# Performance work log

Measured on AMD Instinct MI355X. Metric: run time of the kernel, lower is better.

## Reference

```python
import jax, jax.numpy as jnp
import numpy as np

WIN, STRIDE = 8, 4          # unfold(-1, 8, 4) in FIDSubsequence.forward
HID, FEAT = 128, 30         # action2motion FID classifier: GRU hidden 128, lin1 -> 30
GAMMA = 1.0                 # SoftDTW default gamma
INF = 1e10


def _windows(xyz):
    x = xyz[0]                                   # (J, 3, T)
    T = x.shape[-1]
    nw = (T - WIN) // STRIDE + 1
    idx = jnp.arange(nw)[:, None] * STRIDE + jnp.arange(WIN)[None, :]
    w = x[:, :, idx]
    seq = w.transpose(3, 2, 0, 1)
    return seq.reshape(WIN, nw, -1)


def _gru_layer(xs, Wih, Whh, bih, bhh):
    # xs: (T, B, in); torch GRU gate order r, z, n
    H = Whh.shape[1]
    def step(h, x):
        gi = x @ Wih.T + bih
        gh = h @ Whh.T + bhh
        ir, iz, i_n = jnp.split(gi, 3, -1)
        hr, hz, h_n = jnp.split(gh, 3, -1)
        r = jax.nn.sigmoid(ir + hr)
        z = jax.nn.sigmoid(iz + hz)
        n = jnp.tanh(i_n + r * h_n)
        h_new = (1.0 - z) * n + z * h
        return h_new, h_new
    h0 = jnp.zeros((xs.shape[1], H), xs.dtype)
    _, hs = jax.lax.scan(step, h0, xs)
    return hs                                    # (T, B, H)


def _feats(xyz, Wih1, Whh1, bih1, bhh1, Wih2, Whh2, bih2, bhh2, W1, b1):
    # Batched equivalent of the per-window classifier loop in distance()
    seq = _windows(xyz)                          # (8, nw, 72)
    h1 = _gru_layer(seq, Wih1, Whh1, bih1, bhh1)
    h2 = _gru_layer(h1, Wih2, Whh2, bih2, bhh2)
    return h2[-1] @ W1.T + b1                    # (nw, 30) -- lengths=8 == full window


def _pairwise_sqdist(f1, f2):
    # ((f1 - f2) ** 2).sum(-1) without materializing (n, m, d)
    d = (f1 * f1).sum(-1)[:, None] + (f2 * f2).sum(-1)[None, :] - 2.0 * (f1 @ f2.T)
    return jnp.maximum(d, 0.0)


def _softdtw(D, gamma):
    # anti-diagonal wavefront: A_k[i] = R[i, k-i]
    n, m = D.shape
    rows = jnp.arange(n)
    def step(carry, k):
        A2, A1 = carry
        j = k - rows
        valid = (j >= 0) & (j < m)
        d = D[rows, jnp.clip(j, 0, m - 1)]
        diag = jnp.concatenate([jnp.where(k == 0, 0.0, INF)[None], A2[:-1]])
        up = jnp.concatenate([jnp.full((1,), INF, D.dtype), A1[:-1]])
        smin = -gamma * jax.nn.logsumexp(-jnp.stack([diag, up, A1]) / gamma, axis=0)
        newA = jnp.where(valid, d + smin, INF)
        return (A1, newA), None
    A = jnp.full((n,), INF, D.dtype)
    (_, last), _ = jax.lax.scan(step, (A, A), jnp.arange(n + m - 1))
    return last[-1]                              # R[n-1, m-1]


def setup_inputs() -> dict:
    key = jax.random.key(0)
    ks = jax.random.split(key, 12)
    T, J, IN = 8196, 24, 72
    s = 1.0 / np.sqrt(HID)
    f32 = jnp.float32
    return {
        "x_xyz": jax.random.normal(ks[0], (1, J, 3, T), f32),
        "y_xyz": jax.random.normal(ks[1], (1, J, 3, T), f32),
        "Wih1": jax.random.uniform(ks[2], (3 * HID, IN), f32, -s, s),
        "Whh1": jax.random.uniform(ks[3], (3 * HID, HID), f32, -s, s),
        "bih1": jax.random.uniform(ks[4], (3 * HID,), f32, -s, s),
        "bhh1": jax.random.uniform(ks[5], (3 * HID,), f32, -s, s),
        "Wih2": jax.random.uniform(ks[6], (3 * HID, HID), f32, -s, s),
        "Whh2": jax.random.uniform(ks[7], (3 * HID, HID), f32, -s, s),
        "bih2": jax.random.uniform(ks[8], (3 * HID,), f32, -s, s),
        "bhh2": jax.random.uniform(ks[9], (3 * HID,), f32, -s, s),
        "W1": jax.random.uniform(ks[10], (FEAT, HID), f32, -s, s),
        "b1": jax.random.uniform(ks[11], (FEAT,), f32, -s, s),
    }


def reference(x_xyz, y_xyz, Wih1, Whh1, bih1, bhh1, Wih2, Whh2, bih2, bhh2, W1, b1):
    f1 = _feats(x_xyz, Wih1, Whh1, bih1, bhh1, Wih2, Whh2, bih2, bhh2, W1, b1)
    f2 = _feats(y_xyz, Wih1, Whh1, bih1, bhh1, Wih2, Whh2, bih2, bhh2, W1, b1)
    D = _pairwise_sqdist(f1, f2)                 # (nw, nw)
    return jnp.reshape(_softdtw(D, GAMMA), (1,))
```

## Files before the change

### kernel.cpp

```cpp
#include <hip/hip_runtime.h>
#include <stdint.h>

#define T_LEN 8196
#define LOG2E 1.4426950408889634f
#define LN2   0.6931471805599453f
#define INF2  1.4426950e10f
#define PD_LD 2080
#define PD_OFF 16

__device__ __forceinline__ float fexp2(float x) {
#if __has_builtin(__builtin_amdgcn_exp2f)
    return __builtin_amdgcn_exp2f(x);
#else
    return __expf(x * LN2);
#endif
}
__device__ __forceinline__ float flog2(float x) {
#if __has_builtin(__builtin_amdgcn_logf)
    return __builtin_amdgcn_logf(x);
#else
    return __logf(x) * LOG2E;
#endif
}
__device__ __forceinline__ float sigm(float x) { return 1.0f / (1.0f + __expf(-x)); }
__device__ __forceinline__ float tanh_f(float x) {
    x = fminf(fmaxf(x, -15.0f), 15.0f);
    float e = __expf(2.0f * x);
    return (e - 1.0f) / (e + 1.0f);
}

__global__ void k_prep(const float* __restrict__ Wih1, const float* __restrict__ Whh1,
                       const float* __restrict__ Wih2, const float* __restrict__ Whh2,
                       float* __restrict__ wt) {
    int gid = blockIdx.x * 256 + threadIdx.x;
    if (gid >= 175104) return;
    const float* src;
    int r, K;
    if (gid < 27648)       { r = gid;          K = 72;  src = Wih1; }
    else if (gid < 76800)  { r = gid - 27648;  K = 128; src = Whh1; }
    else if (gid < 125952) { r = gid - 76800;  K = 128; src = Wih2; }
    else                   { r = gid - 125952; K = 128; src = Whh2; }
    int kc   = r / 1536;
    int rem  = r - kc * 1536;
    int gate = rem >> 9;
    int rem2 = rem & 511;
    int u    = rem2 >> 2;
    int ki   = rem2 & 3;
    wt[gid] = src[(gate * 128 + u) * K + kc * 4 + ki];
}

__global__ __launch_bounds__(256)
void k_gru(const float* __restrict__ X, const float* __restrict__ Y,
           const float* __restrict__ wt,
           const float* __restrict__ bih1, const float* __restrict__ bhh1,
           const float* __restrict__ bih2, const float* __restrict__ bhh2,
           const float* __restrict__ W1, const float* __restrict__ b1,
           float* __restrict__ fbuf) {
    __shared__ __align__(16) float xb[72 * 12];
    __shared__ __align__(16) float h1l[128 * 12];
    __shared__ __align__(16) float h2l[128 * 12];

    const int tid = threadIdx.x;
    const int u = tid & 127;
    const int w0 = (tid >> 7) * 4;
    const int bx = blockIdx.x;
    const int seq = bx >> 8;
    const int wbase = (bx & 255) << 3;
    const float* xp = seq ? Y : X;

    const float* wih1 = wt;
    const float* whh1 = wt + 27648;
    const float* wih2 = wt + 76800;
    const float* whh2 = wt + 125952;
    const int u4 = u << 2;

    const float br1  = bih1[u] + bhh1[u];
    const float bz1  = bih1[128 + u] + bhh1[128 + u];
    const float bni1 = bih1[256 + u];
    const float bnh1 = bhh1[256 + u];
    const float br2  = bih2[u] + bhh2[u];
    const float bz2  = bih2[128 + u] + bhh2[128 + u];
    const float bni2 = bih2[256 + u];
    const float bnh2 = bhh2[256 + u];

    float h1r[4], h2r[4];
#pragma unroll
    for (int j = 0; j < 4; ++j) { h1r[j] = 0.f; h2r[j] = 0.f; }
    for (int e = tid; e < 128 * 12; e += 256) { h1l[e] = 0.f; h2l[e] = 0.f; }
    __syncthreads();

    for (int t = 0; t < 8; ++t) {
        for (int e = tid; e < 72 * 8; e += 256) {
            int k = e >> 3, w = e & 7;
            int jj = k / 3, c = k - jj * 3;
            xb[k * 12 + w] = xp[jj * (3 * T_LEN) + c * T_LEN + ((wbase + w) << 2) + t];
        }
        __syncthreads();

        float ar[4], az[4], ai[4], ah[4];
#pragma unroll
        for (int j = 0; j < 4; ++j) { ar[j] = br1; az[j] = bz1; ai[j] = bni1; ah[j] = bnh1; }
#pragma unroll 1
        for (int kc = 0; kc < 18; ++kc) {
            const float4 wr4 = *(const float4*)&wih1[kc * 1536 + u4];
            const float4 wz4 = *(const float4*)&wih1[kc * 1536 + 512 + u4];
            const float4 wn4 = *(const float4*)&wih1[kc * 1536 + 1024 + u4];
            const float wrk[4] = {wr4.x, wr4.y, wr4.z, wr4.w};
            const float wzk[4] = {wz4.x, wz4.y, wz4.z, wz4.w};
            const float wnk[4] = {wn4.x, wn4.y, wn4.z, wn4.w};
#pragma unroll
            for (int ki = 0; ki < 4; ++ki) {
                const float4 x0 = *(const float4*)&xb[(kc * 4 + ki) * 12 + w0];
                float xv[4] = {x0.x, x0.y, x0.z, x0.w};
#pragma unroll
                for (int j = 0; j < 4; ++j) {
                    ar[j] = fmaf(wrk[ki], xv[j], ar[j]);
                    az[j] = fmaf(wzk[ki], xv[j], az[j]);
                    ai[j] = fmaf(wnk[ki], xv[j], ai[j]);
                }
            }
        }
#pragma unroll 1
        for (int kc = 0; kc < 32; ++kc) {
            const float4 wr4 = *(const float4*)&whh1[kc * 1536 + u4];
            const float4 wz4 = *(const float4*)&whh1[kc * 1536 + 512 + u4];
            const float4 wn4 = *(const float4*)&whh1[kc * 1536 + 1024 + u4];
            const float wrk[4] = {wr4.x, wr4.y, wr4.z, wr4.w};
            const float wzk[4] = {wz4.x, wz4.y, wz4.z, wz4.w};
            const float wnk[4] = {wn4.x, wn4.y, wn4.z, wn4.w};
#pragma unroll
            for (int ki = 0; ki < 4; ++ki) {
                const float4 x0 = *(const float4*)&h1l[(kc * 4 + ki) * 12 + w0];
                float xv[4] = {x0.x, x0.y, x0.z, x0.w};
#pragma unroll
                for (int j = 0; j < 4; ++j) {
                    ar[j] = fmaf(wrk[ki], xv[j], ar[j]);
                    az[j] = fmaf(wzk[ki], xv[j], az[j]);
                    ah[j] = fmaf(wnk[ki], xv[j], ah[j]);
                }
            }
        }
        __syncthreads();
#pragma unroll
        for (int j = 0; j < 4; ++j) {
            float r = sigm(ar[j]);
            float z = sigm(az[j]);
            float n = tanh_f(ai[j] + r * ah[j]);
            h1r[j] = (1.f - z) * n + z * h1r[j];
        }
#pragma unroll
        for (int j = 0; j < 4; ++j) h1l[u * 12 + w0 + j] = h1r[j];
        __syncthreads();

#pragma unroll
        for (int j = 0; j < 4; ++j) { ar[j] = br2; az[j] = bz2; ai[j] = bni2; ah[j] = bnh2; }
#pragma unroll 1
        for (int kc = 0; kc < 32; ++kc) {
            const float4 wr4 = *(const float4*)&wih2[kc * 1536 + u4];
            const float4 wz4 = *(const float4*)&wih2[kc * 1536 + 512 + u4];
            const float4 wn4 = *(const float4*)&wih2[kc * 1536 + 1024 + u4];
            const float wrk[4] = {wr4.x, wr4.y, wr4.z, wr4.w};
            const float wzk[4] = {wz4.x, wz4.y, wz4.z, wz4.w};
            const float wnk[4] = {wn4.x, wn4.y, wn4.z, wn4.w};
#pragma unroll
            for (int ki = 0; ki < 4; ++ki) {
                const float4 x0 = *(const float4*)&h1l[(kc * 4 + ki) * 12 + w0];
                float xv[4] = {x0.x, x0.y, x0.z, x0.w};
#pragma unroll
                for (int j = 0; j < 4; ++j) {
                    ar[j] = fmaf(wrk[ki], xv[j], ar[j]);
                    az[j] = fmaf(wzk[ki], xv[j], az[j]);
                    ai[j] = fmaf(wnk[ki], xv[j], ai[j]);
                }
            }
        }
#pragma unroll 1
        for (int kc = 0; kc < 32; ++kc) {
            const float4 wr4 = *(const float4*)&whh2[kc * 1536 + u4];
            const float4 wz4 = *(const float4*)&whh2[kc * 1536 + 512 + u4];
            const float4 wn4 = *(const float4*)&whh2[kc * 1536 + 1024 + u4];
            const float wrk[4] = {wr4.x, wr4.y, wr4.z, wr4.w};
            const float wzk[4] = {wz4.x, wz4.y, wz4.z, wz4.w};
            const float wnk[4] = {wn4.x, wn4.y, wn4.z, wn4.w};
#pragma unroll
            for (int ki = 0; ki < 4; ++ki) {
                const float4 x0 = *(const float4*)&h2l[(kc * 4 + ki) * 12 + w0];
                float xv[4] = {x0.x, x0.y, x0.z, x0.w};
#pragma unroll
                for (int j = 0; j < 4; ++j) {
                    ar[j] = fmaf(wrk[ki], xv[j], ar[j]);
                    az[j] = fmaf(wzk[ki], xv[j], az[j]);
                    ah[j] = fmaf(wnk[ki], xv[j], ah[j]);
                }
            }
        }
        __syncthreads();
#pragma unroll
        for (int j = 0; j < 4; ++j) {
            float r = sigm(ar[j]);
            float z = sigm(az[j]);
            float n = tanh_f(ai[j] + r * ah[j]);
            h2r[j] = (1.f - z) * n + z * h2r[j];
        }
#pragma unroll
        for (int j = 0; j < 4; ++j) h2l[u * 12 + w0 + j] = h2r[j];
        __syncthreads();
    }

    for (int idx = tid; idx < 8 * 30; idx += 256) {
        int w = idx / 30, ff = idx - w * 30;
        float acc = b1[ff];
        for (int k = 0; k < 128; ++k) acc = fmaf(h2l[k * 12 + w], W1[ff * 128 + k], acc);
        fbuf[(seq * 2048 + wbase + w) * 32 + ff] = acc;
    }
}

__global__ __launch_bounds__(256)
void k_pair(const float* __restrict__ fbuf, float* __restrict__ Ep) {
    __shared__ float f1t[64 * 33];
    __shared__ float f2t[64 * 33];
    const int tid = threadIdx.x;
    const int i0 = blockIdx.y * 64, j0 = blockIdx.x * 64;
    for (int e = tid; e < 64 * 32; e += 256) {
        int r = e >> 5, c = e & 31;
        f1t[r * 33 + c] = fbuf[(i0 + r) * 32 + c];
        f2t[r * 33 + c] = fbuf[(2048 + j0 + r) * 32 + c];
    }
    __syncthreads();
    const int tx = tid & 15, ty = tid >> 4;
    float acc[4][4];
#pragma unroll
    for (int r = 0; r < 4; ++r)
#pragma unroll
        for (int c = 0; c < 4; ++c) acc[r][c] = 0.f;
    for (int k = 0; k < 30; ++k) {
        float a[4], b[4];
#pragma unroll
        for (int r = 0; r < 4; ++r) a[r] = f1t[(ty * 4 + r) * 33 + k];
#pragma unroll
        for (int c = 0; c < 4; ++c) b[c] = f2t[(tx * 4 + c) * 33 + k];
#pragma unroll
        for (int r = 0; r < 4; ++r)
#pragma unroll
            for (int c = 0; c < 4; ++c) {
                float d = a[r] - b[c];
                acc[r][c] = fmaf(d, d, acc[r][c]);
            }
    }
#pragma unroll
    for (int r = 0; r < 4; ++r) {
        float4 v = make_float4(__expf(-acc[r][0]), __expf(-acc[r][1]),
                               __expf(-acc[r][2]), __expf(-acc[r][3]));
        *(float4*)&Ep[(size_t)(i0 + ty * 4 + r) * PD_LD + PD_OFF + j0 + tx * 4] = v;
    }
}

#define DTW_GROUP(G, CT)                                                         \
  {                                                                              \
    float inA, inB, dgl;                                                         \
    if (lane == 0) {                                                             \
        inA = sIn[2 * (G)]; inB = sIn[2 * (G) + 1];                              \
        dgl = ((G) == 0) ? carryA : sIn[2 * (G) - 1];                            \
    } else { inA = pA; inB = pB; dgl = dgPrev; }                                 \
    {                                              \
        float mnG = fminf(fminf(inA, inB), dgl);                                 \
        float lim = mnG + 100.f;                                                 \
        if (Sc > lim) {                                                          \
            int ddg = (int)fmaxf(lim - Sc, -2.0e9f);                             \
            W0 = ldexpf(W0, ddg); W1 = ldexpf(W1, ddg);                          \
            W2 = ldexpf(W2, ddg); W3 = ldexpf(W3, ddg);                          \
            Sc = lim;                                                            \
        }                                                                        \
    }                                                                            \
    float ua = fexp2(Sc - inA);                                                  \
    float ub = fexp2(Sc - inB);                                                  \
    float da = fexp2(Sc - dgl);                                                  \
    float eA0 = CT[0][2*(G)],   eA1 = CT[1][2*(G)];                              \
    float eA2 = CT[2][2*(G)],   eA3 = CT[3][2*(G)];                              \
    float eB0 = CT[0][2*(G)+1], eB1 = CT[1][2*(G)+1];                            \
    float eB2 = CT[2][2*(G)+1], eB3 = CT[3][2*(G)+1];                            \
    float oA0 = eA0 * (da + W0);                                                 \
    float oA1 = eA1 * (W0 + W1);                                                 \
    float oA2 = eA2 * (W1 + W2);                                                 \
    float oA3 = eA3 * (W2 + W3);                                                 \
    float a0 = fmaf(eA0, ua, oA0);                                               \
    float a1 = fmaf(eA1, a0, oA1);                                               \
    float a2 = fmaf(eA2, a1, oA2);                                               \
    float a3 = fmaf(eA3, a2, oA3);                                               \
    float oB0 = eB0 * (ua + a0);                                                 \
    float oB1 = eB1 * (a0 + a1);                                                 \
    float oB2 = eB2 * (a1 + a2);                                                 \
    float oB3 = eB3 * (a2 + a3);                                                 \
    float b0 = fmaf(eB0, ub, oB0);                                               \
    float b1 = fmaf(eB1, b0, oB1);                                               \
    float b2 = fmaf(eB2, b1, oB2);                                               \
    float b3 = fmaf(eB3, b2, oB3);                                               \
    W0 = b0; W1 = b1; W2 = b2; W3 = b3;                                          \
    float blogA = fminf(Sc - flog2(a3), INF2);                                   \
    float blogB = fminf(Sc - flog2(b3), INF2);                                   \
    blog[2 * (G)] = blogA; blog[2 * (G) + 1] = blogB;                            \
    float sA = __shfl_up(blogA, 1);                                              \
    float sB = __shfl_up(blogB, 1);                                              \
    dgPrev = pB; pA = sA; pB = sB;                                               \
    mnAcc = fminf(mnAcc, fminf(sA, sB));                                         \
  }

#define DTW_MACRO(CUR, PF, PVC, PVI, M)                                          \
  {                                                                              \
    const int m = (M);                                                           \
    {       \
        int bs = 8 * (m + 2) - 2 * lane;                                         \
        bs = bs < -16 ? -16 : (bs > 2048 ? 2048 : bs);                           \
        _Pragma("unroll")                                                        \
        for (int r = 0; r < 4; ++r) {                                            \
            _Pragma("unroll")                                                    \
            for (int h = 0; h < 4; ++h) {                                        \
                float2 v = *(const float2*)(rp[r] + bs + 2 * h);                 \
                PF[r][2 * h] = v.x; PF[r][2 * h + 1] = v.y;                      \
            }                                                                    \
        }                                                                        \
    }                                                                            \
    if (b > 0 && lane == 0) {            \
        _Pragma("unroll")                                                        \
        for (int u = 0; u < 8; ++u) {                                            \
            int jc = 8 * (m + 3) + u; jc = jc > 2047 ? 2047 : jc;                \
            PVI[u] = __hip_atomic_load(&bIn[jc], __ATOMIC_RELAXED,               \
                                       __HIP_MEMORY_SCOPE_AGENT);                \
        }                                                                        \
    }                                                                            \
    float blog[8];                                                               \
    float mnAcc = INF2;                                                          \
    DTW_GROUP(0, CUR) DTW_GROUP(1, CUR) DTW_GROUP(2, CUR) DTW_GROUP(3, CUR)      \
    carryA = sIn[7];                                                             \
    if (lane == 63) {                                                            \
        if (b < 7) {                                                             \
            _Pragma("unroll")                                                    \
            for (int c = 0; c < 8; ++c) {                                        \
                int j = 8 * m + c - 126;                                         \
                if (j >= 0 && j < 2048) {                                        \
                    uint64_t pk = ((uint64_t)(uint32_t)j << 32) |                \
                                  (uint64_t)__float_as_uint(blog[c]);            \
                    (void)__hip_atomic_exchange(&bOut[j], pk, __ATOMIC_RELAXED,  \
                                                __HIP_MEMORY_SCOPE_AGENT);       \
                }                                                                \
            }                                                                    \
        } else if (m == 271) {                      \
            res = blog[5];                                                       \
        }                                                                        \
    }                                                                            \
    if (b > 0 && lane == 0) {      \
        bool again = false;                                                      \
        _Pragma("unroll")                                                        \
        for (int u = 0; u < 8; ++u) {                                            \
            int jc = 8 * (m + 1) + u; jc = jc > 2047 ? 2047 : jc;                \
            if ((uint32_t)(PVC[u] >> 32) != (uint32_t)jc) again = true;          \
        }                                                                        \
        while (again) {              \
            __builtin_amdgcn_s_sleep(2);                                         \
            _Pragma("unroll")                                                    \
            for (int u = 0; u < 8; ++u) {                                        \
                int jc = 8 * (m + 1) + u; jc = jc > 2047 ? 2047 : jc;            \
                PVC[u] = __hip_atomic_load(&bIn[jc], __ATOMIC_RELAXED,           \
                                           __HIP_MEMORY_SCOPE_AGENT);            \
            }                                                                    \
            again = false;                                                       \
            _Pragma("unroll")                                                    \
            for (int u = 0; u < 8; ++u) {                                        \
                int jc = 8 * (m + 1) + u; jc = jc > 2047 ? 2047 : jc;            \
                if ((uint32_t)(PVC[u] >> 32) != (uint32_t)jc) again = true;      \
            }                                                                    \
        }                                                                        \
        _Pragma("unroll")                                                        \
        for (int u = 0; u < 8; ++u) sIn[u] = __uint_as_float((uint32_t)PVC[u]);  \
    }                                                                            \
    {                                                          \
        float mn = mnAcc;                                                        \
        if (lane == 0) {                                                         \
            if (b > 0) {                                                         \
                mn = sIn[0];                                                     \
                _Pragma("unroll")                                                \
                for (int c = 1; c < 8; ++c) mn = fminf(mn, sIn[c]);              \
            } else {                                                             \
                mn = INF2;                                                       \
            }                                                                    \
        }                                                                        \
        float wmax = fmaxf(fmaxf(W0, W1), fmaxf(W2, W3));                        \
        float Sc_new;                                                            \
        if (wmax > 0.f) {                                                        \
            int e = (int)((__float_as_uint(wmax) >> 23) & 0xFFu) - 127;          \
            Sc_new = fminf(Sc - (float)e, mn + 100.f);                           \
        } else {                                                                 \
            Sc_new = fminf(mn, 1e9f);                                            \
        }                                                                        \
        int dd = (int)fmaxf(fminf(Sc_new - Sc, 999.f), -999.f);                  \
        W0 = ldexpf(W0, dd); W1 = ldexpf(W1, dd);                                \
        W2 = ldexpf(W2, dd); W3 = ldexpf(W3, dd);                                \
        Sc = Sc_new;                                                             \
    }                                                                            \
  }

__global__ __launch_bounds__(64)
void k_dtw(const float* __restrict__ Ep, uint64_t* bndG, float* __restrict__ out) {
    const int b = blockIdx.x;
    const int lane = threadIdx.x;
    const int r0 = b * 256 + lane * 4;
    const uint64_t* bIn = bndG + (size_t)(b - 1) * 2048;
    uint64_t* bOut = bndG + (size_t)b * 2048;

    const float* rp[4];
#pragma unroll
    for (int r = 0; r < 4; ++r) rp[r] = Ep + (size_t)(r0 + r) * PD_LD + PD_OFF;

    float W0 = 0.f, W1 = 0.f, W2 = 0.f, W3 = 0.f;
    float Sc = 0.f;
    float carryA = (b == 0 && lane == 0) ? 0.f : INF2;
    float res = 0.f;
    float pA = INF2, pB = INF2, dgPrev = INF2;
    float sIn[8];
#pragma unroll
    for (int c = 0; c < 8; ++c) sIn[c] = INF2;

    uint64_t pvs0[8], pvs1[8], pvs2[8];
#pragma unroll
    for (int u = 0; u < 8; ++u) { pvs0[u] = 0; pvs1[u] = 0; pvs2[u] = 0; }

    if (b > 0 && lane == 0) {
        {
            uint64_t p = __hip_atomic_load(&bIn[31], __ATOMIC_RELAXED,
                                           __HIP_MEMORY_SCOPE_AGENT);
            while ((uint32_t)(p >> 32) != 31u) {
                __builtin_amdgcn_s_sleep(8);
                p = __hip_atomic_load(&bIn[31], __ATOMIC_RELAXED,
                                      __HIP_MEMORY_SCOPE_AGENT);
            }
        }
        uint64_t pv[8];
        bool again = true;
        while (again) {
#pragma unroll
            for (int u = 0; u < 8; ++u)
                pv[u] = __hip_atomic_load(&bIn[u], __ATOMIC_RELAXED,
                                          __HIP_MEMORY_SCOPE_AGENT);
            again = false;
#pragma unroll
            for (int u = 0; u < 8; ++u)
                if ((uint32_t)(pv[u] >> 32) != (uint32_t)u) again = true;
            if (again) __builtin_amdgcn_s_sleep(2);
        }
        float mn = INF2;
#pragma unroll
        for (int u = 0; u < 8; ++u) {
            sIn[u] = __uint_as_float((uint32_t)pv[u]);
            mn = fminf(mn, sIn[u]);
        }
        Sc = fminf(mn, 1e9f);
#pragma unroll
        for (int u = 0; u < 8; ++u)
            pvs1[u] = __hip_atomic_load(&bIn[8 + u], __ATOMIC_RELAXED,
                                        __HIP_MEMORY_SCOPE_AGENT);
#pragma unroll
        for (int u = 0; u < 8; ++u)
            pvs2[u] = __hip_atomic_load(&bIn[16 + u], __ATOMIC_RELAXED,
                                        __HIP_MEMORY_SCOPE_AGENT);
    }

    float eT0[4][8], eT1[4][8], eT2[4][8];
#pragma unroll
    for (int tt = 0; tt < 2; ++tt) {
        int bs = 8 * tt - 2 * lane;
        bs = bs < -16 ? -16 : bs;
#pragma unroll
        for (int r = 0; r < 4; ++r) {
            float (*dst)[8] = tt ? eT1 : eT0;
#pragma unroll
            for (int h = 0; h < 4; ++h) {
                float2 v = *(const float2*)(rp[r] + bs + 2 * h);
                dst[r][2 * h] = v.x; dst[r][2 * h + 1] = v.y;
            }
        }
    }

    for (int mm = 0; mm < 273; mm += 3) {
        DTW_MACRO(eT0, eT2, pvs1, pvs0, mm);
        DTW_MACRO(eT1, eT0, pvs2, pvs1, mm + 1);
        DTW_MACRO(eT2, eT1, pvs0, pvs2, mm + 2);
    }

    if (b == 7 && lane == 63) out[0] = res * LN2;
}

extern "C" void kernel_launch(void* const* d_in, const int* in_sizes, int n_in,
                              void* d_out, int out_size, void* d_ws, size_t ws_size,
                              hipStream_t stream) {
    const float* X    = (const float*)d_in[0];
    const float* Y    = (const float*)d_in[1];
    const float* Wih1 = (const float*)d_in[2];
    const float* Whh1 = (const float*)d_in[3];
    const float* bih1 = (const float*)d_in[4];
    const float* bhh1 = (const float*)d_in[5];
    const float* Wih2 = (const float*)d_in[6];
    const float* Whh2 = (const float*)d_in[7];
    const float* bih2 = (const float*)d_in[8];
    const float* bhh2 = (const float*)d_in[9];
    const float* W1   = (const float*)d_in[10];
    const float* b1   = (const float*)d_in[11];
    float* out = (float*)d_out;

    float* ws   = (float*)d_ws;
    float* fbuf = ws;
    uint64_t* bndG = (uint64_t*)(ws + 131072);
    float* Ep   = ws + 131072 + 28672;
    float* wt   = Ep + 4259840 - 175104;

    k_prep<<<684, 256, 0, stream>>>(Wih1, Whh1, Wih2, Whh2, wt);
    k_gru<<<512, 256, 0, stream>>>(X, Y, wt, bih1, bhh1, bih2, bhh2, W1, b1, fbuf);
    k_pair<<<dim3(32, 32), 256, 0, stream>>>(fbuf, Ep);
    k_dtw<<<8, 64, 0, stream>>>(Ep, bndG, out);
}
```

Baseline: 757.7 us.

## Add producer wavefront streaming DTW tiles through LDS ring buffer

```diff
diff --git a/kernel.cpp b/kernel.cpp
--- a/kernel.cpp
+++ b/kernel.cpp
@@ -305,21 +305,28 @@
     mnAcc = fminf(mnAcc, fminf(sA, sB));                                         \
   }
 
-#define DTW_MACRO(CUR, PF, PVC, PVI, M)                                          \
+#define DTW_MACRO(PVC, PVI, M)                                                   \
   {                                                                              \
     const int m = (M);                                                           \
-    {       \
-        int bs = 8 * (m + 2) - 2 * lane;                                         \
-        bs = bs < -16 ? -16 : (bs > 2048 ? 2048 : bs);                           \
+    const int bf = m & 3;                                                        \
+    const int q  = m >> 2;                                                       \
+    while (__hip_atomic_load(&flg[bf], __ATOMIC_ACQUIRE,                         \
+                             __HIP_MEMORY_SCOPE_WORKGROUP) != q + 1)             \
+        __builtin_amdgcn_s_sleep(2);                                             \
+    float eT[4][8];                                                              \
+    {                                                                            \
+        const float* cb = &ldsE[bf][lane * 4];                                   \
         _Pragma("unroll")                                                        \
         for (int r = 0; r < 4; ++r) {                                            \
-            _Pragma("unroll")                                                    \
-            for (int h = 0; h < 4; ++h) {                                        \
-                float2 v = *(const float2*)(rp[r] + bs + 2 * h);                 \
-                PF[r][2 * h] = v.x; PF[r][2 * h + 1] = v.y;                      \
-            }                                                                    \
+            float4 lo = *(const float4*)&cb[(2 * r) * 256];                      \
+            float4 hi = *(const float4*)&cb[(2 * r + 1) * 256];                  \
+            eT[r][0]=lo.x; eT[r][1]=lo.y; eT[r][2]=lo.z; eT[r][3]=lo.w;          \
+            eT[r][4]=hi.x; eT[r][5]=hi.y; eT[r][6]=hi.z; eT[r][7]=hi.w;          \
         }                                                                        \
     }                                                                            \
+    if (lane == 0)                                                               \
+        __hip_atomic_store(&cns[bf], q + 1, __ATOMIC_RELEASE,                    \
+                           __HIP_MEMORY_SCOPE_WORKGROUP);                        \
     if (b > 0 && lane == 0) {            \
         _Pragma("unroll")                                                        \
         for (int u = 0; u < 8; ++u) {                                            \
@@ -330,7 +337,7 @@
     }                                                                            \
     float blog[8];                                                               \
     float mnAcc = INF2;                                                          \
-    DTW_GROUP(0, CUR) DTW_GROUP(1, CUR) DTW_GROUP(2, CUR) DTW_GROUP(3, CUR)      \
+    DTW_GROUP(0, eT) DTW_GROUP(1, eT) DTW_GROUP(2, eT) DTW_GROUP(3, eT)          \
     carryA = sIn[7];                                                             \
     if (lane == 63) {                                                            \
         if (b < 7) {                                                             \
@@ -399,17 +406,51 @@
     }                                                                            \
   }
 
-__global__ __launch_bounds__(64)
+__global__ __launch_bounds__(128)
 void k_dtw(const float* __restrict__ Ep, uint64_t* bndG, float* __restrict__ out) {
+    __shared__ __align__(16) float ldsE[4][2048];
+    __shared__ int flg[4];
+    __shared__ int cns[4];
+
     const int b = blockIdx.x;
-    const int lane = threadIdx.x;
-    const int r0 = b * 256 + lane * 4;
+    const int tid = threadIdx.x;
+    const int lane = tid & 63;
+
+    if (tid < 4) { flg[tid] = 0; cns[tid] = 0; }
+    __syncthreads();
+
+    if (tid >= 64) {
+        const int r0 = b * 256 + lane * 4;
+        const float* rp[4];
+#pragma unroll
+        for (int r = 0; r < 4; ++r) rp[r] = Ep + (size_t)(r0 + r) * PD_LD + PD_OFF;
+        for (int m = 0; m <= 272; ++m) {
+            const int bf = m & 3, q = m >> 2;
+            while (__hip_atomic_load(&cns[bf], __ATOMIC_ACQUIRE,
+                                     __HIP_MEMORY_SCOPE_WORKGROUP) != q)
+                __builtin_amdgcn_s_sleep(2);
+            int bs = 8 * m - 2 * lane;
+            bs = bs < -16 ? -16 : (bs > 2048 ? 2048 : bs);
+            float* dst = &ldsE[bf][lane * 4];
+#pragma unroll
+            for (int r = 0; r < 4; ++r) {
+#pragma unroll
+                for (int h = 0; h < 2; ++h) {
+                    float2 v0 = *(const float2*)(rp[r] + bs + 4 * h);
+                    float2 v1 = *(const float2*)(rp[r] + bs + 4 * h + 2);
+                    *(float4*)&dst[(2 * r + h) * 256] =
+                        make_float4(v0.x, v0.y, v1.x, v1.y);
+                }
+            }
+            if (lane == 0)
+                __hip_atomic_store(&flg[bf], q + 1, __ATOMIC_RELEASE,
+                                   __HIP_MEMORY_SCOPE_WORKGROUP);
+        }
+        return;
+    }
+
     const uint64_t* bIn = bndG + (size_t)(b - 1) * 2048;
     uint64_t* bOut = bndG + (size_t)b * 2048;
-
-    const float* rp[4];
-#pragma unroll
-    for (int r = 0; r < 4; ++r) rp[r] = Ep + (size_t)(r0 + r) * PD_LD + PD_OFF;
 
     float W0 = 0.f, W1 = 0.f, W2 = 0.f, W3 = 0.f;
     float Sc = 0.f;
@@ -464,26 +505,10 @@
                                         __HIP_MEMORY_SCOPE_AGENT);
     }
 
-    float eT0[4][8], eT1[4][8], eT2[4][8];
-#pragma unroll
-    for (int tt = 0; tt < 2; ++tt) {
-        int bs = 8 * tt - 2 * lane;
-        bs = bs < -16 ? -16 : bs;
-#pragma unroll
-        for (int r = 0; r < 4; ++r) {
-            float (*dst)[8] = tt ? eT1 : eT0;
-#pragma unroll
-            for (int h = 0; h < 4; ++h) {
-                float2 v = *(const float2*)(rp[r] + bs + 2 * h);
-                dst[r][2 * h] = v.x; dst[r][2 * h + 1] = v.y;
-            }
-        }
-    }
-
     for (int mm = 0; mm < 273; mm += 3) {
-        DTW_MACRO(eT0, eT2, pvs1, pvs0, mm);
-        DTW_MACRO(eT1, eT0, pvs2, pvs1, mm + 1);
-        DTW_MACRO(eT2, eT1, pvs0, pvs2, mm + 2);
+        DTW_MACRO(pvs1, pvs0, mm);
+        DTW_MACRO(pvs2, pvs1, mm + 1);
+        DTW_MACRO(pvs0, pvs2, mm + 2);
     }
 
     if (b == 7 && lane == 63) out[0] = res * LN2;
@@ -515,5 +540,5 @@
     k_prep<<<684, 256, 0, stream>>>(Wih1, Whh1, Wih2, Whh2, wt);
     k_gru<<<512, 256, 0, stream>>>(X, Y, wt, bih1, bhh1, bih2, bhh2, W1, b1, fbuf);
     k_pair<<<dim3(32, 32), 256, 0, stream>>>(fbuf, Ep);
-    k_dtw<<<8, 64, 0, stream>>>(Ep, bndG, out);
-}
+    k_dtw<<<8, 128, 0, stream>>>(Ep, bndG, out);
+}
```

After: 880.3 us. 16.2% more time.
